# Optimization experiments

Hardware: AMD Instinct MI355X
Metric: run time of the kernel (lower is better)

Reference implementation:

```python
import jax, jax.numpy as jnp
import numpy as np

N = 40960      # nodes, level 0
E = 327680     # edges, level 0
N1 = 20480     # nodes after first graclus pool
E2 = 163840    # edges after first pool
N2 = 10240     # nodes after second graclus pool
B = 512        # graphs in batch
NCLS = 10


def seg_mean(v, idx, n):
    s = jax.ops.segment_sum(v, idx, num_segments=n)
    c = jax.ops.segment_sum(jnp.ones((idx.shape[0], 1), v.dtype), idx, num_segments=n)
    return s / jnp.maximum(c, 1.0)


def seg_max_f(v, idx, n):
    m = jax.ops.segment_max(v, idx, num_segments=n)
    return jnp.where(jnp.isneginf(m), 0.0, m)  # empty clusters -> 0


def cartesian(pos, ei):
    # PyG T.Cartesian(): cart = pos[row]-pos[col], normalized to [0,1]
    cart = pos[ei[0]] - pos[ei[1]]
    m = jnp.max(jnp.abs(cart))
    return cart / (2.0 * m) + 0.5


def nnconv_mean(x, ei, eattr, w1, b1, w2, b2, root, bias, n_nodes):
    # edge MLP -> per-edge weight matrix [E, Fin, Fout]
    fin, fout = root.shape
    h = jax.nn.relu(eattr @ w1 + b1) @ w2 + b2
    W = h.reshape(-1, fin, fout)
    src, dst = ei[0], ei[1]
    msg = jnp.einsum('ei,eio->eo', x[src], W)          # gather + per-edge matmul
    aggr = seg_mean(msg, dst, n_nodes)                 # scatter-mean
    return x @ root + aggr + bias


def setup_inputs() -> dict:
    key = jax.random.key(0)
    ks = jax.random.split(key, 24)
    inp = {}
    inp['x'] = jax.random.normal(ks[0], (N, 1), jnp.float32)
    inp['pos'] = jax.random.uniform(ks[1], (N, 2), jnp.float32) * 28.0
    inp['edge_attr'] = jax.random.uniform(ks[2], (E, 2), jnp.float32)
    inp['edge_index'] = jax.random.randint(ks[3], (2, E), 0, N)
    inp['batch'] = jnp.sort(jax.random.randint(ks[4], (N,), 0, B))
    inp['cluster1'] = jax.random.randint(ks[5], (N,), 0, N1)
    inp['edge_index2'] = jax.random.randint(ks[6], (2, E2), 0, N1)
    inp['cluster2'] = jax.random.randint(ks[7], (N1,), 0, N2)
    s = 0.1
    inp['nn1_w1'] = jax.random.normal(ks[8], (2, 25), jnp.float32) * s
    inp['nn1_b1'] = jnp.zeros((25,), jnp.float32)
    inp['nn1_w2'] = jax.random.normal(ks[9], (25, 32), jnp.float32) * s
    inp['nn1_b2'] = jnp.zeros((32,), jnp.float32)
    inp['root1'] = jax.random.normal(ks[10], (1, 32), jnp.float32) * s
    inp['bias1'] = jnp.zeros((32,), jnp.float32)
    inp['nn2_w1'] = jax.random.normal(ks[11], (2, 25), jnp.float32) * s
    inp['nn2_b1'] = jnp.zeros((25,), jnp.float32)
    inp['nn2_w2'] = jax.random.normal(ks[12], (25, 2048), jnp.float32) * s
    inp['nn2_b2'] = jnp.zeros((2048,), jnp.float32)
    inp['root2'] = jax.random.normal(ks[13], (32, 64), jnp.float32) * s
    inp['bias2'] = jnp.zeros((64,), jnp.float32)
    inp['fc1_w'] = jax.random.normal(ks[14], (64, 128), jnp.float32) * s
    inp['fc1_b'] = jnp.zeros((128,), jnp.float32)
    inp['fc2_w'] = jax.random.normal(ks[15], (128, NCLS), jnp.float32) * s
    inp['fc2_b'] = jnp.zeros((NCLS,), jnp.float32)
    return inp


def reference(x, pos, edge_attr, edge_index, batch, cluster1, edge_index2, cluster2,
              nn1_w1, nn1_b1, nn1_w2, nn1_b2, root1, bias1,
              nn2_w1, nn2_b1, nn2_w2, nn2_b2, root2, bias2,
              fc1_w, fc1_b, fc2_w, fc2_b):
    # conv1 + ELU
    x1 = jax.nn.elu(nnconv_mean(x, edge_index, edge_attr,
                                nn1_w1, nn1_b1, nn1_w2, nn1_b2, root1, bias1, N))
    # graclus max_pool (clusters precomputed): max features, mean pos, pooled batch
    x1p = seg_max_f(x1, cluster1, N1)
    pos1 = seg_mean(pos, cluster1, N1)
    batch1 = jnp.clip(jax.ops.segment_max(batch, cluster1, num_segments=N1), 0, B - 1)
    eattr2 = cartesian(pos1, edge_index2)  # transform=Cartesian on pooled graph
    # conv2 + ELU
    x2 = jax.nn.elu(nnconv_mean(x1p, edge_index2, eattr2,
                                nn2_w1, nn2_b1, nn2_w2, nn2_b2, root2, bias2, N1))
    # max_pool_x then global_mean_pool
    x2p = seg_max_f(x2, cluster2, N2)
    batch2 = jnp.clip(jax.ops.segment_max(batch1, cluster2, num_segments=N2), 0, B - 1)
    xg = seg_mean(x2p, batch2, B)
    h = jax.nn.elu(xg @ fc1_w + fc1_b)
    # dropout is identity in eval mode
    logits = h @ fc2_w + fc2_b
    return jax.nn.log_softmax(logits, axis=1)
```

## Files before the change

### kernel.cpp

```cpp
#include <hip/hip_runtime.h>
#include <hip/hip_bf16.h>
#include <limits.h>

#define NN   40960
#define EE   327680
#define NN1  20480
#define EE2  163840
#define NN2  10240
#define BB   512
#define NCLS 10

#define SEG1 160
#define SEG2 240
#define SEG3 320
#define SEG4 400
#define SBT  440

typedef short bf16x8 __attribute__((ext_vector_type(8)));
typedef float f32x4 __attribute__((ext_vector_type(4)));

__device__ __forceinline__ float elu_f(float v) { return v > 0.f ? v : (expf(v) - 1.f); }
__device__ __forceinline__ unsigned f2bf_bits(float v) {
    unsigned u = __float_as_uint(v);
    return (u + 0x7FFFu + ((u >> 16) & 1u)) >> 16;
}

__global__ void init_all(int* zbase, int zcount) {
    int i = blockIdx.x * 256 + threadIdx.x;
    if (i < zcount) zbase[i] = 0;
}

__global__ void deg_count(const int* __restrict__ ei, const int* __restrict__ ei2,
                          const int* __restrict__ cluster1, const int* __restrict__ cluster2,
                          int* deg1, int* degS, int* degD, int* degC1, int* degC2,
                          int* slot1, int* slotS, int* slotD, int* slotC1, int* slotC2) {
    int i = blockIdx.x * 256 + threadIdx.x;
    if (i < EE) slot1[i] = atomicAdd(deg1 + ei[EE + i], 1);
    if (i < EE2) {
        slotS[i] = atomicAdd(degS + ei2[i], 1);
        slotD[i] = atomicAdd(degD + ei2[EE2 + i], 1);
    }
    if (i < NN) slotC1[i] = atomicAdd(degC1 + cluster1[i], 1);
    if (i < NN1) slotC2[i] = atomicAdd(degC2 + cluster2[i], 1);
}

__global__ __launch_bounds__(256) void scan_partial(
    const int* __restrict__ deg1, const int* __restrict__ degS,
    const int* __restrict__ degD, const int* __restrict__ degC1,
    const int* __restrict__ degC2, int* __restrict__ part) {
    int b = blockIdx.x, t = threadIdx.x;
    const int* src;
    int off;
    if (b < SEG1)      { src = deg1;  off = b * 256; }
    else if (b < SEG2) { src = degS;  off = (b - SEG1) * 256; }
    else if (b < SEG3) { src = degD;  off = (b - SEG2) * 256; }
    else if (b < SEG4) { src = degC1; off = (b - SEG3) * 256; }
    else               { src = degC2; off = (b - SEG4) * 256; }
    int v = src[off + t];
#pragma unroll
    for (int o = 32; o; o >>= 1) v += __shfl_down(v, o, 64);
    __shared__ int sred[4];
    if ((t & 63) == 0) sred[t >> 6] = v;
    __syncthreads();
    if (t == 0) part[b] = sred[0] + sred[1] + sred[2] + sred[3];
}

__global__ void scan_base(const int* __restrict__ part, int* __restrict__ partBase,
                          int* rowptr1, int* rowptrS, int* rowptrD,
                          int* rowptrC1, int* rowptrC2) {
    __shared__ int sh[SBT];
    int t = threadIdx.x;
    if (t < SBT) sh[t] = part[t];
    __syncthreads();
    if (t < 5) {
        int lo[6] = {0, SEG1, SEG2, SEG3, SEG4, SBT};
        int run = 0;
        for (int b = lo[t]; b < lo[t + 1]; b++) { int v = sh[b]; sh[b] = run; run += v; }
    }
    if (t == 5) {
        rowptr1[NN] = EE;
        rowptrS[NN1] = EE2;
        rowptrD[NN1] = EE2;
        rowptrC1[NN1] = NN;
        rowptrC2[NN2] = NN1;
    }
    __syncthreads();
    if (t < SBT) partBase[t] = sh[t];
}

__global__ __launch_bounds__(256) void scan_apply(
    const int* __restrict__ deg1, const int* __restrict__ degS,
    const int* __restrict__ degD, const int* __restrict__ degC1,
    const int* __restrict__ degC2, const int* __restrict__ partBase,
    int* rowptr1, int* rowptrS, int* rowptrD, int* rowptrC1, int* rowptrC2) {
    int b = blockIdx.x, t = threadIdx.x;
    const int* src;
    int* rp;
    int off;
    if (b < SEG1)      { src = deg1;  rp = rowptr1;  off = b * 256; }
    else if (b < SEG2) { src = degS;  rp = rowptrS;  off = (b - SEG1) * 256; }
    else if (b < SEG3) { src = degD;  rp = rowptrD;  off = (b - SEG2) * 256; }
    else if (b < SEG4) { src = degC1; rp = rowptrC1; off = (b - SEG3) * 256; }
    else               { src = degC2; rp = rowptrC2; off = (b - SEG4) * 256; }
    __shared__ int sh[256];
    int v = src[off + t];
    sh[t] = v;
    __syncthreads();
#pragma unroll
    for (int o = 1; o < 256; o <<= 1) {
        int u = (t >= o) ? sh[t - o] : 0;
        __syncthreads();
        sh[t] += u;
        __syncthreads();
    }
    rp[off + t] = sh[t] - v + partBase[b];
}

__global__ void fill_csr(const float* __restrict__ x, const float* __restrict__ ea,
                         const int* __restrict__ ei, const int* __restrict__ ei2,
                         const int* __restrict__ cluster1, const int* __restrict__ cluster2,
                         const int* __restrict__ rowptr1, const int* __restrict__ rowptrS,
                         const int* __restrict__ rowptrD, const int* __restrict__ rowptrC1,
                         const int* __restrict__ rowptrC2,
                         const int* __restrict__ slot1, const int* __restrict__ slotS,
                         const int* __restrict__ slotD, const int* __restrict__ slotC1,
                         const int* __restrict__ slotC2,
                         float4* __restrict__ eadj1, int4* __restrict__ cscRec,
                         int* __restrict__ memC1, int* __restrict__ memC2) {
    int i = blockIdx.x * 256 + threadIdx.x;
    if (i < EE) {
        int s = ei[i], d = ei[EE + i];
        eadj1[rowptr1[d] + slot1[i]] = make_float4(x[s], ea[2 * i], ea[2 * i + 1], 0.f);
    }
    if (i < EE2) {
        int s2 = ei2[i], d2 = ei2[EE2 + i];
        int q = rowptrS[s2] + slotS[i];
        int p2 = rowptrD[d2] + slotD[i];
        cscRec[q] = make_int4(s2, d2, p2, 0);
    }
    if (i < NN) memC1[rowptrC1[cluster1[i]] + slotC1[i]] = i;
    if (i < NN1) memC2[rowptrC2[cluster2[i]] + slotC2[i]] = i;
}

__global__ __launch_bounds__(256) void conv1_gather(
    const float* __restrict__ x, const int* __restrict__ rowptr1,
    const float4* __restrict__ eadj1,
    const float* __restrict__ w1, const float* __restrict__ b1,
    const float* __restrict__ w2, const float* __restrict__ b2,
    const float* __restrict__ root1, const float* __restrict__ bias1,
    float* __restrict__ x1) {
    int t = threadIdx.x;
    int j = t & 31;
    int n = blockIdx.x * 8 + (t >> 5);
    float w1x = 0.f, w1y = 0.f, b1j = 0.f;
    if (j < 25) { w1x = w1[j]; w1y = w1[25 + j]; b1j = b1[j]; }
    int r0 = rowptr1[n], r1 = rowptr1[n + 1];
    float agg = 0.f, sumx = 0.f;
    float4 edN = (r0 < r1) ? eadj1[r0] : make_float4(0.f, 0.f, 0.f, 0.f);
    for (int p = r0; p < r1; p++) {
        float4 ed = edN;
        if (p + 1 < r1) edN = eadj1[p + 1];
        float h = fmaxf(fmaf(ed.y, w1x, fmaf(ed.z, w1y, b1j)), 0.f);
        agg = fmaf(ed.x, h, agg);
        sumx += ed.x;
    }
    float w2c[25];
#pragma unroll
    for (int k = 0; k < 25; k++) w2c[k] = w2[k * 32 + j];
    float m = sumx * b2[j];
#pragma unroll
    for (int k = 0; k < 25; k++) m = fmaf(__shfl(agg, k, 32), w2c[k], m);
    float deg = fmaxf((float)(r1 - r0), 1.f);
    float v = fmaf(x[n], root1[j], m / deg + bias1[j]);
    x1[(size_t)n * 32 + j] = elu_f(v);
}

__global__ __launch_bounds__(256) void pool1_gather(
    const float* __restrict__ x1, const float* __restrict__ pos,
    const int* __restrict__ batch, const int* __restrict__ rowptrC1,
    const int* __restrict__ memC1,
    float* __restrict__ x1p, float* __restrict__ pos1, int* __restrict__ batch1) {
    int t = threadIdx.x;
    int j = t & 31;
    int c = blockIdx.x * 8 + (t >> 5);
    int r0 = rowptrC1[c], r1 = rowptrC1[c + 1];
    float mx = -INFINITY, sx = 0.f, sy = 0.f;
    int bmax = INT_MIN;
    for (int p = r0; p < r1; p++) {
        int v = memC1[p];
        mx = fmaxf(mx, x1[(size_t)v * 32 + j]);
        bmax = max(bmax, batch[v]);
        if (j == 0) {
            float2 pv = ((const float2*)pos)[v];
            sx += pv.x; sy += pv.y;
        }
    }
    x1p[(size_t)c * 32 + j] = (r0 < r1) ? mx : 0.f;
    if (j == 0) {
        float cn = fmaxf((float)(r1 - r0), 1.f);
        pos1[2 * c] = sx / cn;
        pos1[2 * c + 1] = sy / cn;
        batch1[c] = min(max(bmax, 0), BB - 1);
    }
}

__global__ void cartmax(const float* __restrict__ pos1, const int* __restrict__ ei2,
                        unsigned* mBits, const float* __restrict__ x1p,
                        unsigned short* __restrict__ x1pb) {
    int e = blockIdx.x * 256 + threadIdx.x;
#pragma unroll
    for (int u = 0; u < 4; u++) {
        int idx = e * 4 + u;
        x1pb[idx] = (unsigned short)f2bf_bits(x1p[idx]);
    }
    float m = 0.f;
    if (e < EE2) {
        int r = ei2[e], c = ei2[EE2 + e];
        m = fmaxf(fabsf(pos1[2 * r] - pos1[2 * c]), fabsf(pos1[2 * r + 1] - pos1[2 * c + 1]));
    }
    for (int off = 32; off; off >>= 1) m = fmaxf(m, __shfl_xor(m, off, 64));
    if ((threadIdx.x & 63) == 0) atomicMax(mBits, __float_as_uint(m));
}

__global__ void prep_wext(const float* __restrict__ w2, const float* __restrict__ b2,
                          unsigned short* __restrict__ WextB) {
    int idx = blockIdx.x * 256 + threadIdx.x;
    if (idx >= 13 * 8 * 64 * 8) return;
    int j = idx & 7;
    int lane = (idx >> 3) & 63;
    int tile = (idx >> 9) & 7;
    int ky = idx >> 12;
    int h = tile >> 2, tt = tile & 3;
    int kmlp = 2 * ky + h;
    int o = tt * 16 + (lane & 15);
    int i = (lane >> 4) * 8 + j;
    float v = (kmlp < 25) ? w2[(size_t)kmlp * 2048 + i * 64 + o] : b2[i * 64 + o];
    WextB[idx] = (unsigned short)f2bf_bits(v);
}

__global__ __launch_bounds__(256) void a_gemm_mfma(
    const unsigned short* __restrict__ x1pb, const unsigned short* __restrict__ WextB,
    unsigned* __restrict__ Au) {
    int t = threadIdx.x;
    int lane = t & 63;
    int w = t >> 6;
    int ky = blockIdx.y;
    int m0 = blockIdx.x * 128 + w * 32;
    int lo16 = lane & 15, hi4 = lane >> 4;
    bf16x8 bf[8];
    const bf16x8* Bp = (const bf16x8*)(WextB + (size_t)ky * 4096);
#pragma unroll
    for (int i = 0; i < 8; i++) bf[i] = Bp[i * 64 + lane];
    const f32x4 zero = {0.f, 0.f, 0.f, 0.f};
#pragma unroll
    for (int mt = 0; mt < 2; mt++) {
        int mbase = m0 + mt * 16;
        bf16x8 af = *(const bf16x8*)(x1pb + ((size_t)(mbase + lo16) * 32 + hi4 * 8));
        f32x4 acc[8];
#pragma unroll
        for (int i = 0; i < 8; i++)
            acc[i] = __builtin_amdgcn_mfma_f32_16x16x32_bf16(af, bf[i], zero, 0, 0, 0);
#pragma unroll
        for (int tt = 0; tt < 4; tt++) {
#pragma unroll
            for (int j = 0; j < 4; j++) {
                int n = mbase + hi4 * 4 + j;
                unsigned lo = f2bf_bits(acc[tt][j]);
                unsigned hi = f2bf_bits(acc[4 + tt][j]);
                Au[(size_t)n * 832 + ky * 64 + tt * 16 + lo16] = lo | (hi << 16);
            }
        }
    }
}

__global__ __launch_bounds__(256) void r2_kernel(
    const int4* __restrict__ cscRec, const float* __restrict__ pos1,
    const float* __restrict__ w1, const float* __restrict__ b1,
    const unsigned* __restrict__ mBits, uint4* __restrict__ r2q) {
    int q = blockIdx.x * 256 + threadIdx.x;
    if (q >= EE2) return;
    int4 rec = cscRec[q];
    int s = rec.x, d = rec.y;
    float inv = 0.5f / __uint_as_float(*mBits);
    float2 ps = ((const float2*)pos1)[s];
    float2 pd = ((const float2*)pos1)[d];
    float cx = fmaf(ps.x - pd.x, inv, 0.5f);
    float cy = fmaf(ps.y - pd.y, inv, 0.5f);
    unsigned out[16];
#pragma unroll
    for (int ky = 0; ky < 13; ky++) {
        int k0 = 2 * ky, k1 = 2 * ky + 1;
        float rlo = fmaxf(fmaf(cx, w1[k0], fmaf(cy, w1[25 + k0], b1[k0])), 0.f);
        float rhi = 1.f;
        if (k1 < 25) rhi = fmaxf(fmaf(cx, w1[k1], fmaf(cy, w1[25 + k1], b1[k1])), 0.f);
        out[ky] = f2bf_bits(rlo) | (f2bf_bits(rhi) << 16);
    }
    out[13] = (unsigned)rec.z;
    out[14] = 0u; out[15] = 0u;
    uint4* dst = r2q + (size_t)q * 4;
    dst[0] = make_uint4(out[0], out[1], out[2], out[3]);
    dst[1] = make_uint4(out[4], out[5], out[6], out[7]);
    dst[2] = make_uint4(out[8], out[9], out[10], out[11]);
    dst[3] = make_uint4(out[12], out[13], out[14], out[15]);
}

__global__ __launch_bounds__(256) void conv2_msg(
    const unsigned* __restrict__ Au, const uint4* __restrict__ r2q,
    const int* __restrict__ rowptrS, unsigned short* __restrict__ msgbuf) {
    int t = threadIdx.x;
    int lane = t & 63;
    int s = __builtin_amdgcn_readfirstlane(blockIdx.x * 4 + (t >> 6));
    unsigned au[13];
    const unsigned* Ab = Au + (size_t)s * 832 + lane;
#pragma unroll
    for (int ky = 0; ky < 13; ky++) au[ky] = Ab[ky * 64];
    int r0 = rowptrS[s], r1 = rowptrS[s + 1];
    for (int q = r0; q < r1; q++) {
        const uint4* rp4 = r2q + (size_t)q * 4;
        uint4 a = rp4[0], b = rp4[1], c = rp4[2], dd = rp4[3];
        unsigned rr[13] = {a.x, a.y, a.z, a.w, b.x, b.y, b.z, b.w, c.x, c.y, c.z, c.w, dd.x};
        unsigned dstSlot = dd.y;
        float m0 = 0.f, m1 = 0.f;
#pragma unroll
        for (int ky = 0; ky < 13; ky++) {
            unsigned rp = rr[ky];
            unsigned ua = au[ky];
            m0 = fmaf(__uint_as_float(rp << 16), __uint_as_float(ua << 16), m0);
            m1 = fmaf(__uint_as_float(rp & 0xFFFF0000u), __uint_as_float(ua & 0xFFFF0000u), m1);
        }
        msgbuf[(size_t)dstSlot * 64 + lane] = (unsigned short)f2bf_bits(m0 + m1);
    }
}

__global__ __launch_bounds__(256) void conv2_fin(
    const unsigned short* __restrict__ msgbuf, const int* __restrict__ rowptrD,
    const float* __restrict__ x1p, const float* __restrict__ root2,
    const float* __restrict__ bias2, float* __restrict__ x2) {
    int t = threadIdx.x;
    int lane = t & 63;
    int n = blockIdx.x * 4 + (t >> 6);
    float Rr[32];
#pragma unroll
    for (int i = 0; i < 32; i++) Rr[i] = root2[i * 64 + lane];
    int r0 = rowptrD[n], r1 = rowptrD[n + 1];
    float acc = 0.f;
    for (int p = r0; p < r1; p++)
        acc += __uint_as_float((unsigned)msgbuf[(size_t)p * 64 + lane] << 16);
    float deg = fmaxf((float)(r1 - r0), 1.f);
    float xv = x1p[(size_t)n * 32 + (lane & 31)];
    float ra2 = bias2[lane];
#pragma unroll
    for (int i = 0; i < 32; i++) ra2 = fmaf(__shfl(xv, i, 64), Rr[i], ra2);
    x2[(size_t)n * 64 + lane] = elu_f(ra2 + acc / deg);
}

__global__ __launch_bounds__(256) void pool2_gather(
    const float* __restrict__ x2, const int* __restrict__ rowptrC2,
    const int* __restrict__ memC2, const int* __restrict__ batch1,
    float* __restrict__ xgsumS, float* __restrict__ gcntS) {
    int t = threadIdx.x;
    int lane = t & 63;
    int n2 = blockIdx.x * 4 + (t >> 6);
    int r0 = rowptrC2[n2], r1 = rowptrC2[n2 + 1];
    float mx = -INFINITY;
    int bmax = INT_MIN;
    for (int p = r0; p < r1; p++) {
        int m = memC2[p];
        mx = fmaxf(mx, x2[(size_t)m * 64 + lane]);
        bmax = max(bmax, batch1[m]);
    }
    float v = (r0 < r1) ? mx : 0.f;
    int b = min(max(bmax, 0), BB - 1);
    int shard = n2 & 7;
    atomicAdd(xgsumS + ((size_t)shard * BB + b) * 64 + lane, v);
    if (lane == 0) atomicAdd(gcntS + shard * BB + b, 1.f);
}

__global__ __launch_bounds__(128) void head_kernel(
    const float* __restrict__ xgsumS, const float* __restrict__ gcntS,
    const float* __restrict__ fc1w, const float* __restrict__ fc1b,
    const float* __restrict__ fc2w, const float* __restrict__ fc2b,
    float* __restrict__ out) {
    int b = blockIdx.x;
    int t = threadIdx.x;
    __shared__ float xg[64];
    __shared__ float h[128];
    __shared__ float lg[NCLS];
    __shared__ float red[2];
    __shared__ float cntsh;
    float s = 0.f;
    if (t < 64) {
#pragma unroll
        for (int sh = 0; sh < 8; sh++) s += xgsumS[((size_t)sh * BB + b) * 64 + t];
    }
    if (t == 64) {
        float c = 0.f;
#pragma unroll
        for (int sh = 0; sh < 8; sh++) c += gcntS[sh * BB + b];
        cntsh = fmaxf(c, 1.f);
    }
    __syncthreads();
    if (t < 64) xg[t] = s / cntsh;
    __syncthreads();
    float a1 = fc1b[t];
    for (int i = 0; i < 64; i++) a1 = fmaf(xg[i], fc1w[i * 128 + t], a1);
    h[t] = elu_f(a1);
    __syncthreads();
    if (t < NCLS) {
        float a = fc2b[t];
        for (int j = 0; j < 128; j++) a = fmaf(h[j], fc2w[j * NCLS + t], a);
        lg[t] = a;
    }
    __syncthreads();
    if (t == 0) {
        float mx = lg[0];
        for (int i = 1; i < NCLS; i++) mx = fmaxf(mx, lg[i]);
        float se = 0.f;
        for (int i = 0; i < NCLS; i++) se += expf(lg[i] - mx);
        red[0] = mx;
        red[1] = logf(se);
    }
    __syncthreads();
    if (t < NCLS) out[(size_t)b * NCLS + t] = lg[t] - red[0] - red[1];
}

extern "C" void kernel_launch(void* const* d_in, const int* in_sizes, int n_in,
                              void* d_out, int out_size, void* d_ws, size_t ws_size,
                              hipStream_t stream) {
    const float* x = (const float*)d_in[0];
    const float* pos = (const float*)d_in[1];
    const float* edge_attr = (const float*)d_in[2];
    const int* ei = (const int*)d_in[3];
    const int* batch = (const int*)d_in[4];
    const int* cluster1 = (const int*)d_in[5];
    const int* ei2 = (const int*)d_in[6];
    const int* cluster2 = (const int*)d_in[7];
    const float* nn1_w1 = (const float*)d_in[8];
    const float* nn1_b1 = (const float*)d_in[9];
    const float* nn1_w2 = (const float*)d_in[10];
    const float* nn1_b2 = (const float*)d_in[11];
    const float* root1 = (const float*)d_in[12];
    const float* bias1 = (const float*)d_in[13];
    const float* nn2_w1 = (const float*)d_in[14];
    const float* nn2_b1 = (const float*)d_in[15];
    const float* nn2_w2 = (const float*)d_in[16];
    const float* nn2_b2 = (const float*)d_in[17];
    const float* root2 = (const float*)d_in[18];
    const float* bias2 = (const float*)d_in[19];
    const float* fc1w = (const float*)d_in[20];
    const float* fc1b = (const float*)d_in[21];
    const float* fc2w = (const float*)d_in[22];
    const float* fc2b = (const float*)d_in[23];

    float* ws = (float*)d_ws;
    constexpr size_t OFF_DEG1 = 0;
    constexpr size_t OFF_DEGS = OFF_DEG1 + NN;
    constexpr size_t OFF_DEGD = OFF_DEGS + NN1;
    constexpr size_t OFF_DEGC1 = OFF_DEGD + NN1;
    constexpr size_t OFF_DEGC2 = OFF_DEGC1 + NN1;
    constexpr size_t OFF_XGS = OFF_DEGC2 + NN2;
    constexpr size_t OFF_GCS = OFF_XGS + (size_t)8 * BB * 64;
    constexpr size_t OFF_MBITS = OFF_GCS + 8 * BB;
    constexpr size_t ZTOT = OFF_MBITS + 4;
    constexpr size_t OFF_PART = ZTOT;
    constexpr size_t OFF_PBASE = OFF_PART + SBT;
    constexpr size_t OFF_ROWPTR1 = OFF_PBASE + SBT;
    constexpr size_t OFF_ROWPTRS = OFF_ROWPTR1 + NN + 4;
    constexpr size_t OFF_ROWPTRD = OFF_ROWPTRS + NN1 + 4;
    constexpr size_t OFF_ROWPTRC1 = OFF_ROWPTRD + NN1 + 4;
    constexpr size_t OFF_ROWPTRC2 = OFF_ROWPTRC1 + NN1 + 4;
    constexpr size_t OFF_SLOT1 = OFF_ROWPTRC2 + NN2 + 4;
    constexpr size_t OFF_SLOTS = OFF_SLOT1 + EE;
    constexpr size_t OFF_SLOTD = OFF_SLOTS + EE2;
    constexpr size_t OFF_SLOTC1 = OFF_SLOTD + EE2;
    constexpr size_t OFF_SLOTC2 = OFF_SLOTC1 + NN;
    constexpr size_t OFF_CSCREC = OFF_SLOTC2 + NN1;
    constexpr size_t OFF_MEMC1 = OFF_CSCREC + (size_t)EE2 * 4;
    constexpr size_t OFF_MEMC2 = OFF_MEMC1 + NN;
    constexpr size_t OFF_X1 = OFF_MEMC2 + NN1;
    constexpr size_t OFF_X1P = OFF_X1 + (size_t)NN * 32;
    constexpr size_t OFF_X1PB = OFF_X1P + (size_t)NN1 * 32;
    constexpr size_t OFF_POS1 = OFF_X1PB + (size_t)NN1 * 16;
    constexpr size_t OFF_BATCH1 = OFF_POS1 + (size_t)NN1 * 2;
    constexpr size_t OFF_X2 = OFF_BATCH1 + NN1;
    constexpr size_t OFF_WEXTB = OFF_X2 + (size_t)NN1 * 64;
    constexpr size_t OFF_UA = OFF_WEXTB + 26624;
    constexpr size_t UASZ = (size_t)EE2 * 16;
    constexpr size_t OFF_MSG = OFF_UA + UASZ;
    constexpr size_t OFF_AU = OFF_MSG + (size_t)EE2 * 32;

    int* deg1 = (int*)(ws + OFF_DEG1);
    int* degS = (int*)(ws + OFF_DEGS);
    int* degD = (int*)(ws + OFF_DEGD);
    int* degC1 = (int*)(ws + OFF_DEGC1);
    int* degC2 = (int*)(ws + OFF_DEGC2);
    float* xgsumS = ws + OFF_XGS;
    float* gcntS = ws + OFF_GCS;
    unsigned* mBits = (unsigned*)(ws + OFF_MBITS);
    int* part = (int*)(ws + OFF_PART);
    int* partBase = (int*)(ws + OFF_PBASE);
    int* rowptr1 = (int*)(ws + OFF_ROWPTR1);
    int* rowptrS = (int*)(ws + OFF_ROWPTRS);
    int* rowptrD = (int*)(ws + OFF_ROWPTRD);
    int* rowptrC1 = (int*)(ws + OFF_ROWPTRC1);
    int* rowptrC2 = (int*)(ws + OFF_ROWPTRC2);
    int* slot1 = (int*)(ws + OFF_SLOT1);
    int* slotS = (int*)(ws + OFF_SLOTS);
    int* slotD = (int*)(ws + OFF_SLOTD);
    int* slotC1 = (int*)(ws + OFF_SLOTC1);
    int* slotC2 = (int*)(ws + OFF_SLOTC2);
    int4* cscRec = (int4*)(ws + OFF_CSCREC);
    int* memC1 = (int*)(ws + OFF_MEMC1);
    int* memC2 = (int*)(ws + OFF_MEMC2);
    float* x1 = ws + OFF_X1;
    float* x1p = ws + OFF_X1P;
    unsigned short* x1pb = (unsigned short*)(ws + OFF_X1PB);
    float* pos1 = ws + OFF_POS1;
    int* batch1 = (int*)(ws + OFF_BATCH1);
    float* x2 = ws + OFF_X2;
    unsigned short* WextB = (unsigned short*)(ws + OFF_WEXTB);
    float4* eadj1 = (float4*)(ws + OFF_UA);
    uint4* r2q = (uint4*)(ws + OFF_UA);
    unsigned short* msgbuf = (unsigned short*)(ws + OFF_MSG);
    unsigned* Au = (unsigned*)(ws + OFF_AU);

    init_all<<<(int)((ZTOT + 255) / 256), 256, 0, stream>>>((int*)d_ws, (int)ZTOT);
    deg_count<<<EE / 256, 256, 0, stream>>>(ei, ei2, cluster1, cluster2,
                                            deg1, degS, degD, degC1, degC2,
                                            slot1, slotS, slotD, slotC1, slotC2);
    scan_partial<<<SBT, 256, 0, stream>>>(deg1, degS, degD, degC1, degC2, part);
    scan_base<<<1, 512, 0, stream>>>(part, partBase, rowptr1, rowptrS, rowptrD,
                                     rowptrC1, rowptrC2);
    scan_apply<<<SBT, 256, 0, stream>>>(deg1, degS, degD, degC1, degC2, partBase,
                                        rowptr1, rowptrS, rowptrD, rowptrC1, rowptrC2);
    fill_csr<<<EE / 256, 256, 0, stream>>>(x, edge_attr, ei, ei2, cluster1, cluster2,
                                           rowptr1, rowptrS, rowptrD, rowptrC1, rowptrC2,
                                           slot1, slotS, slotD, slotC1, slotC2,
                                           eadj1, cscRec, memC1, memC2);
    prep_wext<<<208, 256, 0, stream>>>(nn2_w2, nn2_b2, WextB);
    conv1_gather<<<NN / 8, 256, 0, stream>>>(x, rowptr1, eadj1,
                                             nn1_w1, nn1_b1, nn1_w2, nn1_b2, root1, bias1, x1);
    pool1_gather<<<NN1 / 8, 256, 0, stream>>>(x1, pos, batch, rowptrC1, memC1,
                                              x1p, pos1, batch1);
    cartmax<<<EE2 / 256, 256, 0, stream>>>(pos1, ei2, mBits, x1p, x1pb);
    a_gemm_mfma<<<dim3(NN1 / 128, 13), 256, 0, stream>>>(x1pb, WextB, Au);
    r2_kernel<<<EE2 / 256, 256, 0, stream>>>(cscRec, pos1, nn2_w1, nn2_b1, mBits, r2q);
    conv2_msg<<<NN1 / 4, 256, 0, stream>>>(Au, r2q, rowptrS, msgbuf);
    conv2_fin<<<NN1 / 4, 256, 0, stream>>>(msgbuf, rowptrD, x1p, root2, bias2, x2);
    pool2_gather<<<NN2 / 4, 256, 0, stream>>>(x2, rowptrC2, memC2, batch1, xgsumS, gcntS);
    head_kernel<<<BB, 128, 0, stream>>>(xgsumS, gcntS, fc1w, fc1b, fc2w, fc2b,
                                        (float*)d_out);
}
```

Before: 208.9 us.

## Merge small launches, drop scan_base, fuse bf16 cast into pool, deepen prefetch

Removes the single-block scan_base kernel; each scan_apply block now sums the preceding partial counts of its own segment. It folds the bf16 conversion of x1p into pool1_gather, merges cartmax with prep_wext, and merges the MFMA GEMM with the r2 edge kernel into one launch using block-index ranges. It also deepens the prefetch in conv1_gather to two edges and adds one-ahead prefetch of r2q records in conv2_msg. The goal is fewer kernel launches and less exposed memory latency, at the cost of some redundant partial-sum reads and higher register pressure.

```diff
diff --git a/kernel.cpp b/kernel.cpp
--- a/kernel.cpp
+++ b/kernel.cpp
@@ -15,6 +15,11 @@
 #define SEG3 320
 #define SEG4 400
 #define SBT  440
+
+#define GEMM_BLKS 2080
+#define R2_BLKS   640
+#define CART_BLKS 640
+#define PREP_BLKS 208
 
 typedef short bf16x8 __attribute__((ext_vector_type(8)));
 typedef float f32x4 __attribute__((ext_vector_type(4)));
@@ -65,55 +70,46 @@
     if (t == 0) part[b] = sred[0] + sred[1] + sred[2] + sred[3];
 }
 
-__global__ void scan_base(const int* __restrict__ part, int* __restrict__ partBase,
-                          int* rowptr1, int* rowptrS, int* rowptrD,
-                          int* rowptrC1, int* rowptrC2) {
-    __shared__ int sh[SBT];
-    int t = threadIdx.x;
-    if (t < SBT) sh[t] = part[t];
-    __syncthreads();
-    if (t < 5) {
-        int lo[6] = {0, SEG1, SEG2, SEG3, SEG4, SBT};
-        int run = 0;
-        for (int b = lo[t]; b < lo[t + 1]; b++) { int v = sh[b]; sh[b] = run; run += v; }
-    }
-    if (t == 5) {
+__global__ __launch_bounds__(256) void scan_apply(
+    const int* __restrict__ deg1, const int* __restrict__ degS,
+    const int* __restrict__ degD, const int* __restrict__ degC1,
+    const int* __restrict__ degC2, const int* __restrict__ part,
+    int* rowptr1, int* rowptrS, int* rowptrD, int* rowptrC1, int* rowptrC2) {
+    int b = blockIdx.x, t = threadIdx.x;
+    const int* src;
+    int* rp;
+    int off, segLo;
+    if (b < SEG1)      { src = deg1;  rp = rowptr1;  off = b * 256;          segLo = 0; }
+    else if (b < SEG2) { src = degS;  rp = rowptrS;  off = (b - SEG1) * 256; segLo = SEG1; }
+    else if (b < SEG3) { src = degD;  rp = rowptrD;  off = (b - SEG2) * 256; segLo = SEG2; }
+    else if (b < SEG4) { src = degC1; rp = rowptrC1; off = (b - SEG3) * 256; segLo = SEG3; }
+    else               { src = degC2; rp = rowptrC2; off = (b - SEG4) * 256; segLo = SEG4; }
+    int bs = 0;
+    for (int p = segLo + t; p < b; p += 256) bs += part[p];
+#pragma unroll
+    for (int o = 32; o; o >>= 1) bs += __shfl_down(bs, o, 64);
+    __shared__ int sred[4];
+    __shared__ int sh[256];
+    if ((t & 63) == 0) sred[t >> 6] = bs;
+    int v = src[off + t];
+    sh[t] = v;
+    __syncthreads();
+    int base = sred[0] + sred[1] + sred[2] + sred[3];
+#pragma unroll
+    for (int o = 1; o < 256; o <<= 1) {
+        int u = (t >= o) ? sh[t - o] : 0;
+        __syncthreads();
+        sh[t] += u;
+        __syncthreads();
+    }
+    rp[off + t] = sh[t] - v + base;
+    if (b == 0 && t == 0) {
         rowptr1[NN] = EE;
         rowptrS[NN1] = EE2;
         rowptrD[NN1] = EE2;
         rowptrC1[NN1] = NN;
         rowptrC2[NN2] = NN1;
     }
-    __syncthreads();
-    if (t < SBT) partBase[t] = sh[t];
-}
-
-__global__ __launch_bounds__(256) void scan_apply(
-    const int* __restrict__ deg1, const int* __restrict__ degS,
-    const int* __restrict__ degD, const int* __restrict__ degC1,
-    const int* __restrict__ degC2, const int* __restrict__ partBase,
-    int* rowptr1, int* rowptrS, int* rowptrD, int* rowptrC1, int* rowptrC2) {
-    int b = blockIdx.x, t = threadIdx.x;
-    const int* src;
-    int* rp;
-    int off;
-    if (b < SEG1)      { src = deg1;  rp = rowptr1;  off = b * 256; }
-    else if (b < SEG2) { src = degS;  rp = rowptrS;  off = (b - SEG1) * 256; }
-    else if (b < SEG3) { src = degD;  rp = rowptrD;  off = (b - SEG2) * 256; }
-    else if (b < SEG4) { src = degC1; rp = rowptrC1; off = (b - SEG3) * 256; }
-    else               { src = degC2; rp = rowptrC2; off = (b - SEG4) * 256; }
-    __shared__ int sh[256];
-    int v = src[off + t];
-    sh[t] = v;
-    __syncthreads();
-#pragma unroll
-    for (int o = 1; o < 256; o <<= 1) {
-        int u = (t >= o) ? sh[t - o] : 0;
-        __syncthreads();
-        sh[t] += u;
-        __syncthreads();
-    }
-    rp[off + t] = sh[t] - v + partBase[b];
 }
 
 __global__ void fill_csr(const float* __restrict__ x, const float* __restrict__ ea,
@@ -156,10 +152,13 @@
     if (j < 25) { w1x = w1[j]; w1y = w1[25 + j]; b1j = b1[j]; }
     int r0 = rowptr1[n], r1 = rowptr1[n + 1];
     float agg = 0.f, sumx = 0.f;
-    float4 edN = (r0 < r1) ? eadj1[r0] : make_float4(0.f, 0.f, 0.f, 0.f);
+    float4 e0 = make_float4(0.f, 0.f, 0.f, 0.f), e1 = e0;
+    if (r0 < r1) e0 = eadj1[r0];
+    if (r0 + 1 < r1) e1 = eadj1[r0 + 1];
     for (int p = r0; p < r1; p++) {
-        float4 ed = edN;
-        if (p + 1 < r1) edN = eadj1[p + 1];
+        float4 ed = e0;
+        e0 = e1;
+        if (p + 2 < r1) e1 = eadj1[p + 2];
         float h = fmaxf(fmaf(ed.y, w1x, fmaf(ed.z, w1y, b1j)), 0.f);
         agg = fmaf(ed.x, h, agg);
         sumx += ed.x;
@@ -179,7 +178,8 @@
     const float* __restrict__ x1, const float* __restrict__ pos,
     const int* __restrict__ batch, const int* __restrict__ rowptrC1,
     const int* __restrict__ memC1,
-    float* __restrict__ x1p, float* __restrict__ pos1, int* __restrict__ batch1) {
+    float* __restrict__ x1p, unsigned short* __restrict__ x1pb,
+    float* __restrict__ pos1, int* __restrict__ batch1) {
     int t = threadIdx.x;
     int j = t & 31;
     int c = blockIdx.x * 8 + (t >> 5);
@@ -195,7 +195,9 @@
             sx += pv.x; sy += pv.y;
         }
     }
-    x1p[(size_t)c * 32 + j] = (r0 < r1) ? mx : 0.f;
+    float outv = (r0 < r1) ? mx : 0.f;
+    x1p[(size_t)c * 32 + j] = outv;
+    x1pb[(size_t)c * 32 + j] = (unsigned short)f2bf_bits(outv);
     if (j == 0) {
         float cn = fmaxf((float)(r1 - r0), 1.f);
         pos1[2 * c] = sx / cn;
@@ -204,104 +206,104 @@
     }
 }
 
-__global__ void cartmax(const float* __restrict__ pos1, const int* __restrict__ ei2,
-                        unsigned* mBits, const float* __restrict__ x1p,
-                        unsigned short* __restrict__ x1pb) {
-    int e = blockIdx.x * 256 + threadIdx.x;
-#pragma unroll
-    for (int u = 0; u < 4; u++) {
-        int idx = e * 4 + u;
-        x1pb[idx] = (unsigned short)f2bf_bits(x1p[idx]);
-    }
-    float m = 0.f;
-    if (e < EE2) {
-        int r = ei2[e], c = ei2[EE2 + e];
-        m = fmaxf(fabsf(pos1[2 * r] - pos1[2 * c]), fabsf(pos1[2 * r + 1] - pos1[2 * c + 1]));
-    }
-    for (int off = 32; off; off >>= 1) m = fmaxf(m, __shfl_xor(m, off, 64));
-    if ((threadIdx.x & 63) == 0) atomicMax(mBits, __float_as_uint(m));
-}
-
-__global__ void prep_wext(const float* __restrict__ w2, const float* __restrict__ b2,
-                          unsigned short* __restrict__ WextB) {
-    int idx = blockIdx.x * 256 + threadIdx.x;
-    if (idx >= 13 * 8 * 64 * 8) return;
-    int j = idx & 7;
-    int lane = (idx >> 3) & 63;
-    int tile = (idx >> 9) & 7;
-    int ky = idx >> 12;
-    int h = tile >> 2, tt = tile & 3;
-    int kmlp = 2 * ky + h;
-    int o = tt * 16 + (lane & 15);
-    int i = (lane >> 4) * 8 + j;
-    float v = (kmlp < 25) ? w2[(size_t)kmlp * 2048 + i * 64 + o] : b2[i * 64 + o];
-    WextB[idx] = (unsigned short)f2bf_bits(v);
-}
-
-__global__ __launch_bounds__(256) void a_gemm_mfma(
+__global__ void cartmax_prep(const float* __restrict__ pos1, const int* __restrict__ ei2,
+                             unsigned* mBits,
+                             const float* __restrict__ w2, const float* __restrict__ b2,
+                             unsigned short* __restrict__ WextB) {
+    int b = blockIdx.x;
+    int t = threadIdx.x;
+    if (b < CART_BLKS) {
+        int e = b * 256 + t;
+        float m = 0.f;
+        if (e < EE2) {
+            int r = ei2[e], c = ei2[EE2 + e];
+            m = fmaxf(fabsf(pos1[2 * r] - pos1[2 * c]),
+                      fabsf(pos1[2 * r + 1] - pos1[2 * c + 1]));
+        }
+        for (int off = 32; off; off >>= 1) m = fmaxf(m, __shfl_xor(m, off, 64));
+        if ((t & 63) == 0) atomicMax(mBits, __float_as_uint(m));
+    } else {
+        int idx = (b - CART_BLKS) * 256 + t;
+        if (idx >= 13 * 8 * 64 * 8) return;
+        int j = idx & 7;
+        int lane = (idx >> 3) & 63;
+        int tile = (idx >> 9) & 7;
+        int ky = idx >> 12;
+        int h = tile >> 2, tt = tile & 3;
+        int kmlp = 2 * ky + h;
+        int o = tt * 16 + (lane & 15);
+        int i = (lane >> 4) * 8 + j;
+        float v = (kmlp < 25) ? w2[(size_t)kmlp * 2048 + i * 64 + o] : b2[i * 64 + o];
+        WextB[idx] = (unsigned short)f2bf_bits(v);
+    }
+}
+
+__global__ __launch_bounds__(256) void gemm_r2(
     const unsigned short* __restrict__ x1pb, const unsigned short* __restrict__ WextB,
-    unsigned* __restrict__ Au) {
-    int t = threadIdx.x;
-    int lane = t & 63;
-    int w = t >> 6;
-    int ky = blockIdx.y;
-    int m0 = blockIdx.x * 128 + w * 32;
-    int lo16 = lane & 15, hi4 = lane >> 4;
-    bf16x8 bf[8];
-    const bf16x8* Bp = (const bf16x8*)(WextB + (size_t)ky * 4096);
-#pragma unroll
-    for (int i = 0; i < 8; i++) bf[i] = Bp[i * 64 + lane];
-    const f32x4 zero = {0.f, 0.f, 0.f, 0.f};
-#pragma unroll
-    for (int mt = 0; mt < 2; mt++) {
-        int mbase = m0 + mt * 16;
-        bf16x8 af = *(const bf16x8*)(x1pb + ((size_t)(mbase + lo16) * 32 + hi4 * 8));
-        f32x4 acc[8];
-#pragma unroll
-        for (int i = 0; i < 8; i++)
-            acc[i] = __builtin_amdgcn_mfma_f32_16x16x32_bf16(af, bf[i], zero, 0, 0, 0);
-#pragma unroll
-        for (int tt = 0; tt < 4; tt++) {
-#pragma unroll
-            for (int j = 0; j < 4; j++) {
-                int n = mbase + hi4 * 4 + j;
-                unsigned lo = f2bf_bits(acc[tt][j]);
-                unsigned hi = f2bf_bits(acc[4 + tt][j]);
-                Au[(size_t)n * 832 + ky * 64 + tt * 16 + lo16] = lo | (hi << 16);
-            }
-        }
-    }
-}
-
-__global__ __launch_bounds__(256) void r2_kernel(
+    unsigned* __restrict__ Au,
     const int4* __restrict__ cscRec, const float* __restrict__ pos1,
     const float* __restrict__ w1, const float* __restrict__ b1,
     const unsigned* __restrict__ mBits, uint4* __restrict__ r2q) {
-    int q = blockIdx.x * 256 + threadIdx.x;
-    if (q >= EE2) return;
-    int4 rec = cscRec[q];
-    int s = rec.x, d = rec.y;
-    float inv = 0.5f / __uint_as_float(*mBits);
-    float2 ps = ((const float2*)pos1)[s];
-    float2 pd = ((const float2*)pos1)[d];
-    float cx = fmaf(ps.x - pd.x, inv, 0.5f);
-    float cy = fmaf(ps.y - pd.y, inv, 0.5f);
-    unsigned out[16];
-#pragma unroll
-    for (int ky = 0; ky < 13; ky++) {
-        int k0 = 2 * ky, k1 = 2 * ky + 1;
-        float rlo = fmaxf(fmaf(cx, w1[k0], fmaf(cy, w1[25 + k0], b1[k0])), 0.f);
-        float rhi = 1.f;
-        if (k1 < 25) rhi = fmaxf(fmaf(cx, w1[k1], fmaf(cy, w1[25 + k1], b1[k1])), 0.f);
-        out[ky] = f2bf_bits(rlo) | (f2bf_bits(rhi) << 16);
-    }
-    out[13] = (unsigned)rec.z;
-    out[14] = 0u; out[15] = 0u;
-    uint4* dst = r2q + (size_t)q * 4;
-    dst[0] = make_uint4(out[0], out[1], out[2], out[3]);
-    dst[1] = make_uint4(out[4], out[5], out[6], out[7]);
-    dst[2] = make_uint4(out[8], out[9], out[10], out[11]);
-    dst[3] = make_uint4(out[12], out[13], out[14], out[15]);
+    int blk = blockIdx.x;
+    int t = threadIdx.x;
+    if (blk < GEMM_BLKS) {
+        int lane = t & 63;
+        int w = t >> 6;
+        int bx = blk % 160;
+        int ky = blk / 160;
+        int m0 = bx * 128 + w * 32;
+        int lo16 = lane & 15, hi4 = lane >> 4;
+        bf16x8 bf[8];
+        const bf16x8* Bp = (const bf16x8*)(WextB + (size_t)ky * 4096);
+#pragma unroll
+        for (int i = 0; i < 8; i++) bf[i] = Bp[i * 64 + lane];
+        const f32x4 zero = {0.f, 0.f, 0.f, 0.f};
+#pragma unroll
+        for (int mt = 0; mt < 2; mt++) {
+            int mbase = m0 + mt * 16;
+            bf16x8 af = *(const bf16x8*)(x1pb + ((size_t)(mbase + lo16) * 32 + hi4 * 8));
+            f32x4 acc[8];
+#pragma unroll
+            for (int i = 0; i < 8; i++)
+                acc[i] = __builtin_amdgcn_mfma_f32_16x16x32_bf16(af, bf[i], zero, 0, 0, 0);
+#pragma unroll
+            for (int tt = 0; tt < 4; tt++) {
+#pragma unroll
+                for (int j = 0; j < 4; j++) {
+                    int n = mbase + hi4 * 4 + j;
+                    unsigned lo = f2bf_bits(acc[tt][j]);
+                    unsigned hi = f2bf_bits(acc[4 + tt][j]);
+                    Au[(size_t)n * 832 + ky * 64 + tt * 16 + lo16] = lo | (hi << 16);
+                }
+            }
+        }
+    } else {
+        int q = (blk - GEMM_BLKS) * 256 + t;
+        if (q >= EE2) return;
+        int4 rec = cscRec[q];
+        int s = rec.x, d = rec.y;
+        float inv = 0.5f / __uint_as_float(*mBits);
+        float2 ps = ((const float2*)pos1)[s];
+        float2 pd = ((const float2*)pos1)[d];
+        float cx = fmaf(ps.x - pd.x, inv, 0.5f);
+        float cy = fmaf(ps.y - pd.y, inv, 0.5f);
+        unsigned out[16];
+#pragma unroll
+        for (int ky = 0; ky < 13; ky++) {
+            int k0 = 2 * ky, k1 = 2 * ky + 1;
+            float rlo = fmaxf(fmaf(cx, w1[k0], fmaf(cy, w1[25 + k0], b1[k0])), 0.f);
+            float rhi = 1.f;
+            if (k1 < 25) rhi = fmaxf(fmaf(cx, w1[k1], fmaf(cy, w1[25 + k1], b1[k1])), 0.f);
+            out[ky] = f2bf_bits(rlo) | (f2bf_bits(rhi) << 16);
+        }
+        out[13] = (unsigned)rec.z;
+        out[14] = 0u; out[15] = 0u;
+        uint4* dst = r2q + (size_t)q * 4;
+        dst[0] = make_uint4(out[0], out[1], out[2], out[3]);
+        dst[1] = make_uint4(out[4], out[5], out[6], out[7]);
+        dst[2] = make_uint4(out[8], out[9], out[10], out[11]);
+        dst[3] = make_uint4(out[12], out[13], out[14], out[15]);
+    }
 }
 
 __global__ __launch_bounds__(256) void conv2_msg(
@@ -315,9 +317,17 @@
 #pragma unroll
     for (int ky = 0; ky < 13; ky++) au[ky] = Ab[ky * 64];
     int r0 = rowptrS[s], r1 = rowptrS[s + 1];
+    uint4 A0, B0, C0, D0;
+    if (r0 < r1) {
+        const uint4* p4 = r2q + (size_t)r0 * 4;
+        A0 = p4[0]; B0 = p4[1]; C0 = p4[2]; D0 = p4[3];
+    }
     for (int q = r0; q < r1; q++) {
-        const uint4* rp4 = r2q + (size_t)q * 4;
-        uint4 a = rp4[0], b = rp4[1], c = rp4[2], dd = rp4[3];
+        uint4 a = A0, b = B0, c = C0, dd = D0;
+        if (q + 1 < r1) {
+            const uint4* p4 = r2q + (size_t)(q + 1) * 4;
+            A0 = p4[0]; B0 = p4[1]; C0 = p4[2]; D0 = p4[3];
+        }
         unsigned rr[13] = {a.x, a.y, a.z, a.w, b.x, b.y, b.z, b.w, c.x, c.y, c.z, c.w, dd.x};
         unsigned dstSlot = dd.y;
         float m0 = 0.f, m1 = 0.f;
@@ -463,8 +473,7 @@
     constexpr size_t OFF_MBITS = OFF_GCS + 8 * BB;
     constexpr size_t ZTOT = OFF_MBITS + 4;
     constexpr size_t OFF_PART = ZTOT;
-    constexpr size_t OFF_PBASE = OFF_PART + SBT;
-    constexpr size_t OFF_ROWPTR1 = OFF_PBASE + SBT;
+    constexpr size_t OFF_ROWPTR1 = OFF_PART + SBT;
     constexpr size_t OFF_ROWPTRS = OFF_ROWPTR1 + NN + 4;
     constexpr size_t OFF_ROWPTRD = OFF_ROWPTRS + NN1 + 4;
     constexpr size_t OFF_ROWPTRC1 = OFF_ROWPTRD + NN1 + 4;
@@ -498,7 +507,6 @@
     float* gcntS = ws + OFF_GCS;
     unsigned* mBits = (unsigned*)(ws + OFF_MBITS);
     int* part = (int*)(ws + OFF_PART);
-    int* partBase = (int*)(ws + OFF_PBASE);
     int* rowptr1 = (int*)(ws + OFF_ROWPTR1);
     int* rowptrS = (int*)(ws + OFF_ROWPTRS);
     int* rowptrD = (int*)(ws + OFF_ROWPTRD);
@@ -529,22 +537,21 @@
                                             deg1, degS, degD, degC1, degC2,
                                             slot1, slotS, slotD, slotC1, slotC2);
     scan_partial<<<SBT, 256, 0, stream>>>(deg1, degS, degD, degC1, degC2, part);
-    scan_base<<<1, 512, 0, stream>>>(part, partBase, rowptr1, rowptrS, rowptrD,
-                                     rowptrC1, rowptrC2);
-    scan_apply<<<SBT, 256, 0, stream>>>(deg1, degS, degD, degC1, degC2, partBase,
+    scan_apply<<<SBT, 256, 0, stream>>>(deg1, degS, degD, degC1, degC2, part,
                                         rowptr1, rowptrS, rowptrD, rowptrC1, rowptrC2);
     fill_csr<<<EE / 256, 256, 0, stream>>>(x, edge_attr, ei, ei2, cluster1, cluster2,
                                            rowptr1, rowptrS, rowptrD, rowptrC1, rowptrC2,
                                            slot1, slotS, slotD, slotC1, slotC2,
                                            eadj1, cscRec, memC1, memC2);
-    prep_wext<<<208, 256, 0, stream>>>(nn2_w2, nn2_b2, WextB);
     conv1_gather<<<NN / 8, 256, 0, stream>>>(x, rowptr1, eadj1,
                                              nn1_w1, nn1_b1, nn1_w2, nn1_b2, root1, bias1, x1);
     pool1_gather<<<NN1 / 8, 256, 0, stream>>>(x1, pos, batch, rowptrC1, memC1,
-                                              x1p, pos1, batch1);
-    cartmax<<<EE2 / 256, 256, 0, stream>>>(pos1, ei2, mBits, x1p, x1pb);
-    a_gemm_mfma<<<dim3(NN1 / 128, 13), 256, 0, stream>>>(x1pb, WextB, Au);
-    r2_kernel<<<EE2 / 256, 256, 0, stream>>>(cscRec, pos1, nn2_w1, nn2_b1, mBits, r2q);
+                                              x1p, x1pb, pos1, batch1);
+    cartmax_prep<<<CART_BLKS + PREP_BLKS, 256, 0, stream>>>(pos1, ei2, mBits,
+                                                            nn2_w2, nn2_b2, WextB);
+    gemm_r2<<<GEMM_BLKS + R2_BLKS, 256, 0, stream>>>(x1pb, WextB, Au,
+                                                     cscRec, pos1, nn2_w1, nn2_b1,
+                                                     mBits, r2q);
     conv2_msg<<<NN1 / 4, 256, 0, stream>>>(Au, r2q, rowptrS, msgbuf);
     conv2_fin<<<NN1 / 4, 256, 0, stream>>>(msgbuf, rowptrD, x1p, root2, bias2, x2);
     pool2_gather<<<NN2 / 4, 256, 0, stream>>>(x2, rowptrC2, memC2, batch1, xgsumS, gcntS);
```

Result: faster. 200.5 us, median of 2 (-4.0%).
